# Kernel tuning notes

Measured on AMD Instinct MI355X. Metric: run time of the kernel, lower is better.

Reference implementation:

```python
import jax, jax.numpy as jnp
import numpy as np

MARGIN = 1.0

def setup_inputs() -> dict:
    key = jax.random.key(0)
    k1, k2 = jax.random.split(key)
    output = jax.random.normal(k1, (4096, 200), dtype=jnp.float32)
    labels = jax.random.randint(k2, (4096, 200), 0, 2, dtype=jnp.int32)
    return {"output": output, "labels": labels}

def reference(output, labels):
    # output: [B, L] scores; labels: [B, L] in {0,1}
    lab = labels.astype(output.dtype)
    # all positive-negative pairs per sample: diff[b,i,j] = pred_i - pred_j
    diff = output[:, :, None] - output[:, None, :]              # [B, L, L]
    pair_mask = lab[:, :, None] * (1.0 - lab[:, None, :])        # 1 where i is pos, j is neg
    # margin_ranking_loss with y=1: max(0, margin - (pos - neg))
    hinge = jnp.maximum(0.0, MARGIN - diff) * pair_mask          # [B, L, L]
    n_pos = jnp.sum(lab, axis=1)                                 # [B]
    n_neg = lab.shape[1] - n_pos
    n_pairs = n_pos * n_neg
    per_sample_sum = jnp.sum(hinge, axis=(1, 2))                 # [B]
    # reduction='mean' over the n_pos*n_neg pairs of each sample
    per_sample = jnp.where(n_pairs > 0, per_sample_sum / jnp.maximum(n_pairs, 1.0), 0.0)
    # original sums per-sample losses and divides by batch size
    return jnp.sum(per_sample) / output.shape[0]
```

## Files before the change

kernel.cpp:

```cpp
#include <hip/hip_runtime.h>


constexpr int L  = 200;
constexpr int LQ = L / 4;
constexpr float MARGIN = 1.0f;

__global__ __launch_bounds__(64) void rerank_per_sample(
    const float* __restrict__ scores,
    const int*   __restrict__ labels,
    float*       __restrict__ per_sample)
{
    __shared__ float posv[L + 8];
    __shared__ float negv[L + 8];

    const int b    = blockIdx.x;
    const int lane = threadIdx.x;

    float4 sv = make_float4(0.f, 0.f, 0.f, 0.f);
    int4   lv = make_int4(0, 0, 0, 0);
    const bool act = lane < LQ;
    if (act) {
        sv = ((const float4*)(scores + (long)b * L))[lane];
        lv = ((const int4*)(labels + (long)b * L))[lane];
    }
    const float ev[4] = {sv.x, sv.y, sv.z, sv.w};
    const int   lb[4] = {lv.x, lv.y, lv.z, lv.w};

    const unsigned long long lower = (1ull << lane) - 1ull;
    int npos = 0, nneg = 0;
#pragma unroll
    for (int j = 0; j < 4; ++j) {
        const bool isp = act && (lb[j] != 0);
        const bool isn = act && (lb[j] == 0);
        const unsigned long long mp = __ballot(isp);
        const unsigned long long mn = __ballot(isn);
        if (isp) posv[npos + __popcll(mp & lower)] = ev[j];
        if (isn) negv[nneg + __popcll(mn & lower)] = ev[j];
        npos += __popcll(mp);
        nneg += __popcll(mn);
    }

    const int nneg4 = (nneg + 3) & ~3;
    if (lane < nneg4 - nneg) negv[nneg + lane] = -3.0e38f;
    __syncthreads();

    float acc = 0.0f;
    const float4* nv = (const float4*)negv;
    const int nq = nneg4 >> 2;
    for (int i = lane; i < npos; i += 64) {
        const float c = MARGIN - posv[i];
        float a0 = 0.f, a1 = 0.f, a2 = 0.f, a3 = 0.f;
        for (int j = 0; j < nq; ++j) {
            float4 n = nv[j];
            a0 += fmaxf(c + n.x, 0.0f);
            a1 += fmaxf(c + n.y, 0.0f);
            a2 += fmaxf(c + n.z, 0.0f);
            a3 += fmaxf(c + n.w, 0.0f);
        }
        acc += (a0 + a1) + (a2 + a3);
    }

    for (int o = 32; o; o >>= 1) acc += __shfl_down(acc, o, 64);
    if (lane == 0) {
        const float np = (float)npos * (float)nneg;
        per_sample[b] = (np > 0.0f) ? (acc / np) : 0.0f;
    }
}

__global__ __launch_bounds__(256) void rerank_reduce(
    const float* __restrict__ per_sample,
    float*       __restrict__ out,
    int n)
{
    __shared__ float wsum[4];
    const int tid = threadIdx.x;
    float acc = 0.0f;
    const float4* pv = (const float4*)per_sample;
    for (int i = tid; i < (n >> 2); i += 256) {
        float4 v = pv[i];
        acc += (v.x + v.y) + (v.z + v.w);
    }
    for (int o = 32; o; o >>= 1) acc += __shfl_down(acc, o, 64);
    if ((tid & 63) == 0) wsum[tid >> 6] = acc;
    __syncthreads();
    if (tid == 0) out[0] = ((wsum[0] + wsum[1]) + (wsum[2] + wsum[3])) / (float)n;
}

extern "C" void kernel_launch(void* const* d_in, const int* in_sizes, int n_in,
                              void* d_out, int out_size, void* d_ws, size_t ws_size,
                              hipStream_t stream)
{
    const float* scores = (const float*)d_in[0];
    const int*   labels = (const int*)d_in[1];
    float*       out    = (float*)d_out;
    float*       ws     = (float*)d_ws;

    const int B = in_sizes[0] / L;

    rerank_per_sample<<<B, 64, 0, stream>>>(scores, labels, ws);
    rerank_reduce<<<1, 256, 0, stream>>>(ws, out, B);
}
```

Before: 14.15 us.

## Fuse per-sample loss and batch reduction via atomicAdd, four samples per block

Measured after the change: 26.28 us. +85.8%, slower.

```diff
diff --git a/kernel.cpp b/kernel.cpp
--- a/kernel.cpp
+++ b/kernel.cpp
@@ -5,16 +5,20 @@
 constexpr int LQ = L / 4;
 constexpr float MARGIN = 1.0f;
 
-__global__ __launch_bounds__(64) void rerank_per_sample(
+__global__ __launch_bounds__(256) void rerank_fused(
     const float* __restrict__ scores,
     const int*   __restrict__ labels,
-    float*       __restrict__ per_sample)
+    float*       __restrict__ out,
+    float invB)
 {
-    __shared__ float posv[L + 8];
-    __shared__ float negv[L + 8];
+    __shared__ __align__(16) float posv[4][208];
+    __shared__ __align__(16) float negv[4][208];
+    __shared__ float wpart[4];
 
-    const int b    = blockIdx.x;
-    const int lane = threadIdx.x;
+    const int tid  = threadIdx.x;
+    const int w    = tid >> 6;
+    const int lane = tid & 63;
+    const int b    = blockIdx.x * 4 + w;
 
     float4 sv = make_float4(0.f, 0.f, 0.f, 0.f);
     int4   lv = make_int4(0, 0, 0, 0);
@@ -34,21 +38,21 @@
         const bool isn = act && (lb[j] == 0);
         const unsigned long long mp = __ballot(isp);
         const unsigned long long mn = __ballot(isn);
-        if (isp) posv[npos + __popcll(mp & lower)] = ev[j];
-        if (isn) negv[nneg + __popcll(mn & lower)] = ev[j];
+        if (isp) posv[w][npos + __popcll(mp & lower)] = ev[j];
+        if (isn) negv[w][nneg + __popcll(mn & lower)] = ev[j];
         npos += __popcll(mp);
         nneg += __popcll(mn);
     }
 
     const int nneg4 = (nneg + 3) & ~3;
-    if (lane < nneg4 - nneg) negv[nneg + lane] = -3.0e38f;
+    if (lane < nneg4 - nneg) negv[w][nneg + lane] = -3.0e38f;
     __syncthreads();
 
     float acc = 0.0f;
-    const float4* nv = (const float4*)negv;
+    const float4* nv = (const float4*)&negv[w][0];
     const int nq = nneg4 >> 2;
     for (int i = lane; i < npos; i += 64) {
-        const float c = MARGIN - posv[i];
+        const float c = MARGIN - posv[w][i];
         float a0 = 0.f, a1 = 0.f, a2 = 0.f, a3 = 0.f;
         for (int j = 0; j < nq; ++j) {
             float4 n = nv[j];
@@ -63,27 +67,13 @@
     for (int o = 32; o; o >>= 1) acc += __shfl_down(acc, o, 64);
     if (lane == 0) {
         const float np = (float)npos * (float)nneg;
-        per_sample[b] = (np > 0.0f) ? (acc / np) : 0.0f;
+        wpart[w] = (np > 0.0f) ? (acc / np) * invB : 0.0f;
     }
-}
-
-__global__ __launch_bounds__(256) void rerank_reduce(
-    const float* __restrict__ per_sample,
-    float*       __restrict__ out,
-    int n)
-{
-    __shared__ float wsum[4];
-    const int tid = threadIdx.x;
-    float acc = 0.0f;
-    const float4* pv = (const float4*)per_sample;
-    for (int i = tid; i < (n >> 2); i += 256) {
-        float4 v = pv[i];
-        acc += (v.x + v.y) + (v.z + v.w);
+    __syncthreads();
+    if (tid == 0) {
+        const float s = (wpart[0] + wpart[1]) + (wpart[2] + wpart[3]);
+        atomicAdd(out, s);
     }
-    for (int o = 32; o; o >>= 1) acc += __shfl_down(acc, o, 64);
-    if ((tid & 63) == 0) wsum[tid >> 6] = acc;
-    __syncthreads();
-    if (tid == 0) out[0] = ((wsum[0] + wsum[1]) + (wsum[2] + wsum[3])) / (float)n;
 }
 
 extern "C" void kernel_launch(void* const* d_in, const int* in_sizes, int n_in,
@@ -93,10 +83,9 @@
     const float* scores = (const float*)d_in[0];
     const int*   labels = (const int*)d_in[1];
     float*       out    = (float*)d_out;
-    float*       ws     = (float*)d_ws;
 
     const int B = in_sizes[0] / L;
 
-    rerank_per_sample<<<B, 64, 0, stream>>>(scores, labels, ws);
-    rerank_reduce<<<1, 256, 0, stream>>>(ws, out, B);
+    hipMemsetAsync(out, 0, sizeof(float), stream);
+    rerank_fused<<<B / 4, 256, 0, stream>>>(scores, labels, out, 1.0f / (float)B);
 }
```
